# Kernel optimization log

Hardware: AMD Instinct MI355X
Metric: run time of the kernel (lower is better)

## Reference

```python
import jax, jax.numpy as jnp
import numpy as np

# ---- config (mirrors cfg in __init__) ----
XB = (-51.2, 51.2, 0.2)
YB = (-51.2, 51.2, 0.2)
ZB = (-10.0, 10.0, 20.0)
C_BEV = 64
BN_EPS = 1e-5

DX = jnp.array([XB[2], YB[2], ZB[2]], jnp.float32)
BX = jnp.array([XB[0] + XB[2] / 2, YB[0] + YB[2] / 2, ZB[0] + ZB[2] / 2], jnp.float32)
NX = (int((XB[1] - XB[0]) / XB[2]), int((YB[1] - YB[0]) / YB[2]), int((ZB[1] - ZB[0]) / ZB[2]))  # (512, 512, 1)


def setup_inputs() -> dict:
    key = jax.random.key(0)
    k1, k2, k3, k4 = jax.random.split(key, 4)
    B, N = 4, 100000
    xy = jax.random.uniform(k1, (B, N, 2), jnp.float32, -54.0, 54.0)   # some points out of bounds
    z = jax.random.uniform(k2, (B, N, 1), jnp.float32, -3.0, 3.0)
    inten = jax.random.uniform(k3, (B, N, 1), jnp.float32)
    points = jnp.concatenate([xy, z, inten], axis=-1)
    W = jax.random.normal(k4, (4, C_BEV), jnp.float32) * 0.5
    b = jnp.zeros((C_BEV,), jnp.float32)
    gamma = jnp.ones((C_BEV,), jnp.float32)
    beta = jnp.zeros((C_BEV,), jnp.float32)
    return {"points": points, "W": W, "b": b, "gamma": gamma, "beta": beta}


def reference(points, W, b, gamma, beta):
    B, N, _ = points.shape
    nx, ny, nz = NX
    p = points.reshape(-1, 4)                      # (B*N, 4)

    # PFN: Linear + BatchNorm1d (training-mode batch stats, biased var) + ReLU
    h = p @ W + b                                  # (B*N, C)
    mu = jnp.mean(h, axis=0)
    var = jnp.var(h, axis=0)
    feat = jax.nn.relu(gamma * (h - mu) * jax.lax.rsqrt(var + BN_EPS) + beta)

    # grid coords: torch .long() truncates toward zero; jnp astype(int) does too
    coords = ((p[:, :3] - (BX - DX / 2.0)) / DX).astype(jnp.int32)
    kept = ((coords[:, 0] >= 0) & (coords[:, 0] < nx)
            & (coords[:, 1] >= 0) & (coords[:, 1] < ny)
            & (coords[:, 2] >= 0) & (coords[:, 2] < nz))

    batch_ix = jnp.repeat(jnp.arange(B, dtype=jnp.int32), N)
    ranks = (batch_ix * (nx * ny * nz)
             + coords[:, 0] + coords[:, 1] * nx + coords[:, 2] * (nx * ny))

    # invalid points -> sentinel bucket (jit-safe replacement for boolean filtering).
    # segment_sum per unique rank == the sort + QuickCumsum trick + scatter-assign.
    flat = B * nx * ny * nz
    ranks = jnp.where(kept, ranks, flat)
    feat = jnp.where(kept[:, None], feat, 0.0)
    bev = jax.ops.segment_sum(feat, ranks, num_segments=flat + 1)[:flat]  # (flat, C)

    bev = bev.reshape(B, nz, ny, nx, C_BEV)
    bev = jnp.transpose(bev, (0, 4, 1, 2, 3)).sum(axis=2)  # (B, C, ny, nx)
    return bev
```

## Files before the change

### kernel.cpp

```cpp
#include <hip/hip_runtime.h>


#define NXG 512
#define NYXG (512 * 512)
#define CB 64
#define SBLK 256
#define YCH 16
#define CAP 384

typedef float f32x4 __attribute__((ext_vector_type(4)));

__device__ __forceinline__ int coord_mul5(float x, float offx) {
    float t = x - offx;
    asm volatile("" : "+v"(t));
    float q = t * 5.0f;
    asm volatile("" : "+v"(q));
    return (int)q;
}

__global__ void zero_ints(int* __restrict__ p, int n) {
    int i = blockIdx.x * blockDim.x + threadIdx.x;
    if (i < n) p[i] = 0;
}

__global__ void zero_kernel(float4* __restrict__ p, long n4) {
    long i = (long)blockIdx.x * blockDim.x + threadIdx.x;
    long stride = (long)gridDim.x * blockDim.x;
    float4 z = make_float4(0.f, 0.f, 0.f, 0.f);
    for (; i < n4; i += stride) p[i] = z;
}

__global__ void stats_reorder(const float4* __restrict__ pts, const float* __restrict__ W,
                              double* __restrict__ S_part, int* __restrict__ cursor,
                              float4* __restrict__ pts_s, int M, int Nper) {
    __shared__ float4 tile[256];
    __shared__ double sh1[256], sh2[256];
    int t = threadIdx.x;
    int lane = t & 63;
    int wv = t >> 6;
    float w0 = W[lane], w1 = W[64 + lane], w2 = W[128 + lane], w3 = W[192 + lane];
    const float offx = -51.1f - 0.1f;
    double s1 = 0.0, s2 = 0.0;

    int chunk = (M + gridDim.x - 1) / gridDim.x;
    int base = blockIdx.x * chunk;
    int end = base + chunk; if (end > M) end = M;

    for (int i0 = base; i0 < end; i0 += 256) {
        int n = end - i0; if (n > 256) n = 256;
        __syncthreads();
        if (t < n) {
            float4 p = pts[i0 + t];
            tile[t] = p;
            int cx = coord_mul5(p.x, offx);
            int cy = coord_mul5(p.y, offx);
            if (cx >= 0 && cx < NXG && cy >= 0 && cy < NXG) {
                int b = (i0 + t) / Nper;
                int row = (b << 9) | cy;
                int idx = atomicAdd(&cursor[row], 1);
                if (idx < CAP) pts_s[(size_t)row * CAP + idx] = p;
            }
        }
        __syncthreads();
        int j0 = wv * 64, j1 = j0 + 64; if (j1 > n) j1 = n;
        for (int j = j0; j < j1; ++j) {
            float4 p = tile[j];
            float q = p.x * w0 + p.y * w1 + p.z * w2 + p.w * w3;
            double qd = (double)q;
            s1 += qd;
            s2 += qd * qd;
        }
    }
    sh1[t] = s1;
    sh2[t] = s2;
    __syncthreads();
    if (t < 64) {
        int c = t;
        S_part[(long)blockIdx.x * 128 + c] =
            (sh1[c] + sh1[64 + c]) + (sh1[128 + c] + sh1[192 + c]);
        S_part[(long)blockIdx.x * 128 + 64 + c] =
            (sh2[c] + sh2[64 + c]) + (sh2[128 + c] + sh2[192 + c]);
    }
}

__global__ void reduce_finalize(const double* __restrict__ S_part,
                                const float* __restrict__ gamma, const float* __restrict__ beta,
                                float* __restrict__ AB, double invM) {
    __shared__ double sh[4][128];
    __shared__ double tot[128];
    int t = threadIdx.x;
    int g = t >> 7, tt = t & 127;
    const double* base = S_part + (long)g * 64 * 128 + tt;
    double a0 = 0.0, a1 = 0.0, a2 = 0.0, a3 = 0.0;
#pragma unroll
    for (int b = 0; b < 64; b += 4) {
        a0 += base[(long)(b + 0) * 128];
        a1 += base[(long)(b + 1) * 128];
        a2 += base[(long)(b + 2) * 128];
        a3 += base[(long)(b + 3) * 128];
    }
    sh[g][tt] = (a0 + a1) + (a2 + a3);
    __syncthreads();
    if (t < 128) tot[t] = (sh[0][t] + sh[1][t]) + (sh[2][t] + sh[3][t]);
    __syncthreads();
    if (t < 64) {
        double mu = tot[t] * invM;
        double var = tot[64 + t] * invM - mu * mu;
        double sc = (double)gamma[t] / sqrt(var + 1e-5);
        AB[t] = (float)sc;
        AB[64 + t] = (float)((double)beta[t] - mu * sc);
    }
}

__global__ __launch_bounds__(256) void gather_out(
    const float4* __restrict__ pts_s, const float* __restrict__ W,
    const float* __restrict__ AB, const int* __restrict__ cursor,
    float* __restrict__ out) {
    __shared__ float acc[YCH][NXG];
    __shared__ int cnts[YCH];
    int t = threadIdx.x;
    int c = blockIdx.x & 63;
    int yc = (blockIdx.x >> 6) & 31;
    int b = blockIdx.x >> 11;
    int rowbase = (b << 9) + (yc << 4);

    f32x4* az = (f32x4*)acc;
#pragma unroll
    for (int j = t; j < YCH * NXG / 4; j += 256) az[j] = (f32x4)(0.f);
    if (t < YCH) {
        int cc = cursor[rowbase + t];
        cnts[t] = cc > CAP ? CAP : cc;
    }

    float w0 = W[c], w1 = W[64 + c], w2 = W[128 + c], w3 = W[192 + c];
    float A = AB[c], Bc = AB[64 + c];
    const float offx = -51.1f - 0.1f;
    __syncthreads();

    for (int rr = 0; rr < YCH; ++rr) {
        int cnt = cnts[rr];
        const float4* src = pts_s + (size_t)(rowbase + rr) * CAP;
        for (int i = t; i < cnt; i += 256) {
            float4 p = src[i];
            int cx = coord_mul5(p.x, offx);
            float q = p.x * w0 + p.y * w1 + p.z * w2 + p.w * w3;
            float f = fmaxf(q * A + Bc, 0.f);
            atomicAdd(&acc[rr][cx], f);
        }
    }
    __syncthreads();

    f32x4* o4 = (f32x4*)(out + ((size_t)(b * CB + c) * NXG + (yc << 4)) * NXG);
#pragma unroll
    for (int j = t; j < YCH * NXG / 4; j += 256)
        __builtin_nontemporal_store(az[j], &o4[j]);
}

__global__ void stats_only(const float4* __restrict__ pts, const float* __restrict__ W,
                           double* __restrict__ S_part, int M) {
    __shared__ float4 tile[256];
    __shared__ double sh1[256], sh2[256];
    int t = threadIdx.x, lane = t & 63, wv = t >> 6;
    float w0 = W[lane], w1 = W[64 + lane], w2 = W[128 + lane], w3 = W[192 + lane];
    double s1 = 0.0, s2 = 0.0;
    int chunk = (M + gridDim.x - 1) / gridDim.x;
    int base = blockIdx.x * chunk;
    int end = base + chunk; if (end > M) end = M;
    for (int i0 = base; i0 < end; i0 += 256) {
        int n = end - i0; if (n > 256) n = 256;
        __syncthreads();
        if (t < n) tile[t] = pts[i0 + t];
        __syncthreads();
        int j0 = wv * 64, j1 = j0 + 64; if (j1 > n) j1 = n;
        for (int j = j0; j < j1; ++j) {
            float4 p = tile[j];
            float q = p.x * w0 + p.y * w1 + p.z * w2 + p.w * w3;
            double qd = (double)q;
            s1 += qd; s2 += qd * qd;
        }
    }
    sh1[t] = s1; sh2[t] = s2;
    __syncthreads();
    if (t < 64) {
        int c = t;
        S_part[(long)blockIdx.x * 128 + c] =
            (sh1[c] + sh1[64 + c]) + (sh1[128 + c] + sh1[192 + c]);
        S_part[(long)blockIdx.x * 128 + 64 + c] =
            (sh2[c] + sh2[64 + c]) + (sh2[128 + c] + sh2[192 + c]);
    }
}

__global__ void scatter_direct(const float4* __restrict__ pts, const float* __restrict__ W,
                               const float* __restrict__ AB, float* __restrict__ out,
                               int M, int Nper) {
    int lane = threadIdx.x & 63;
    int wid = blockIdx.x * (blockDim.x >> 6) + (threadIdx.x >> 6);
    int nw = gridDim.x * (blockDim.x >> 6);
    float w0 = W[lane], w1 = W[64 + lane], w2 = W[128 + lane], w3 = W[192 + lane];
    float A = AB[lane], Bc = AB[64 + lane];
    const float offx = -51.1f - 0.1f;
    for (int i = wid; i < M; i += nw) {
        float4 p = pts[i];
        int cx = coord_mul5(p.x, offx);
        int cy = coord_mul5(p.y, offx);
        if (cx < 0 || cx >= NXG || cy < 0 || cy >= NXG) continue;
        int b = i / Nper;
        float q = p.x * w0 + p.y * w1 + p.z * w2 + p.w * w3;
        float f = fmaxf(q * A + Bc, 0.f);
        atomicAdd(&out[((long)(b * CB + lane) * NXG + cy) * NXG + cx], f);
    }
}

extern "C" void kernel_launch(void* const* d_in, const int* in_sizes, int n_in,
                              void* d_out, int out_size, void* d_ws, size_t ws_size,
                              hipStream_t stream) {
    const float4* pts = (const float4*)d_in[0];
    const float* W = (const float*)d_in[1];
    const float* gamma = (const float*)d_in[3];
    const float* beta = (const float*)d_in[4];
    float* out = (float*)d_out;

    int M = in_sizes[0] / 4;
    int B = out_size / (CB * NYXG);
    int Nper = M / B;
    int NROWS = B * 512;

    char* wsb = (char*)d_ws;
    float* AB = (float*)(wsb + 1024);
    double* S_part = (double*)(wsb + 2048);

    size_t off = 2048 + (size_t)SBLK * 128 * sizeof(double);
    int* cursor = (int*)(wsb + off);     off += (size_t)NROWS * 4;
    off = (off + 255) & ~(size_t)255;
    float4* pts_s = (float4*)(wsb + off);
    off += (size_t)NROWS * CAP * 16;
    size_t need = off;

    if (ws_size >= need) {
        zero_ints<<<(NROWS + 255) / 256, 256, 0, stream>>>(cursor, NROWS);
        stats_reorder<<<SBLK, 256, 0, stream>>>(pts, W, S_part, cursor, pts_s, M, Nper);
        reduce_finalize<<<1, 512, 0, stream>>>(S_part, gamma, beta, AB, 1.0 / (double)M);
        gather_out<<<B * 32 * 64, 256, 0, stream>>>(pts_s, W, AB, cursor, out);
    } else {
        zero_kernel<<<2048, 256, 0, stream>>>((float4*)out, (long)out_size / 4);
        stats_only<<<SBLK, 256, 0, stream>>>(pts, W, S_part, M);
        reduce_finalize<<<1, 512, 0, stream>>>(S_part, gamma, beta, AB, 1.0 / (double)M);
        scatter_direct<<<2048, 256, 0, stream>>>(pts, W, AB, out, M, Nper);
    }
}
```

Baseline: 203.3 us.

## Compute BatchNorm stats from input moments instead of per-channel projections

```diff
diff --git a/kernel.cpp b/kernel.cpp
--- a/kernel.cpp
+++ b/kernel.cpp
@@ -4,7 +4,7 @@
 #define NXG 512
 #define NYXG (512 * 512)
 #define CB 64
-#define SBLK 256
+#define NST 512
 #define YCH 16
 #define CAP 384
 
@@ -30,82 +30,81 @@
     for (; i < n4; i += stride) p[i] = z;
 }
 
-__global__ void stats_reorder(const float4* __restrict__ pts, const float* __restrict__ W,
-                              double* __restrict__ S_part, int* __restrict__ cursor,
-                              float4* __restrict__ pts_s, int M, int Nper) {
-    __shared__ float4 tile[256];
-    __shared__ double sh1[256], sh2[256];
-    int t = threadIdx.x;
-    int lane = t & 63;
-    int wv = t >> 6;
-    float w0 = W[lane], w1 = W[64 + lane], w2 = W[128 + lane], w3 = W[192 + lane];
+__global__ __launch_bounds__(256) void stats_reorder(
+    const float4* __restrict__ pts, double* __restrict__ S_part,
+    int* __restrict__ cursor, float4* __restrict__ pts_s, int M, int Nper) {
+    double mm[14];
+#pragma unroll
+    for (int v = 0; v < 14; ++v) mm[v] = 0.0;
+
     const float offx = -51.1f - 0.1f;
-    double s1 = 0.0, s2 = 0.0;
-
-    int chunk = (M + gridDim.x - 1) / gridDim.x;
-    int base = blockIdx.x * chunk;
-    int end = base + chunk; if (end > M) end = M;
-
-    for (int i0 = base; i0 < end; i0 += 256) {
-        int n = end - i0; if (n > 256) n = 256;
-        __syncthreads();
-        if (t < n) {
-            float4 p = pts[i0 + t];
-            tile[t] = p;
-            int cx = coord_mul5(p.x, offx);
-            int cy = coord_mul5(p.y, offx);
-            if (cx >= 0 && cx < NXG && cy >= 0 && cy < NXG) {
-                int b = (i0 + t) / Nper;
-                int row = (b << 9) | cy;
-                int idx = atomicAdd(&cursor[row], 1);
-                if (idx < CAP) pts_s[(size_t)row * CAP + idx] = p;
-            }
+    int i = blockIdx.x * blockDim.x + threadIdx.x;
+    int stride = gridDim.x * blockDim.x;
+    for (; i < M; i += stride) {
+        float4 p = pts[i];
+        int cx = coord_mul5(p.x, offx);
+        int cy = coord_mul5(p.y, offx);
+        if (cx >= 0 && cx < NXG && cy >= 0 && cy < NXG) {
+            int b = i / Nper;
+            int row = (b << 9) | cy;
+            int idx = atomicAdd(&cursor[row], 1);
+            if (idx < CAP) pts_s[(size_t)row * CAP + idx] = p;
         }
-        __syncthreads();
-        int j0 = wv * 64, j1 = j0 + 64; if (j1 > n) j1 = n;
-        for (int j = j0; j < j1; ++j) {
-            float4 p = tile[j];
-            float q = p.x * w0 + p.y * w1 + p.z * w2 + p.w * w3;
-            double qd = (double)q;
-            s1 += qd;
-            s2 += qd * qd;
-        }
-    }
-    sh1[t] = s1;
-    sh2[t] = s2;
+        double x = p.x, y = p.y, z = p.z, w = p.w;
+        mm[0] += x; mm[1] += y; mm[2] += z; mm[3] += w;
+        mm[4] += x * x; mm[5] += x * y; mm[6] += x * z; mm[7] += x * w;
+        mm[8] += y * y; mm[9] += y * z; mm[10] += y * w;
+        mm[11] += z * z; mm[12] += z * w; mm[13] += w * w;
+    }
+
+#pragma unroll
+    for (int o = 32; o > 0; o >>= 1) {
+#pragma unroll
+        for (int v = 0; v < 14; ++v) mm[v] += __shfl_down(mm[v], o);
+    }
+    __shared__ double sh[4][14];
+    int lane = threadIdx.x & 63, wv = threadIdx.x >> 6;
+    if (lane == 0) {
+#pragma unroll
+        for (int v = 0; v < 14; ++v) sh[wv][v] = mm[v];
+    }
+    __syncthreads();
+    int t = threadIdx.x;
+    if (t < 14)
+        S_part[(long)blockIdx.x * 16 + t] =
+            (sh[0][t] + sh[1][t]) + (sh[2][t] + sh[3][t]);
+}
+
+__global__ void reduce_finalize(const double* __restrict__ S_part,
+                                const float* __restrict__ W,
+                                const float* __restrict__ gamma, const float* __restrict__ beta,
+                                float* __restrict__ AB, double invM, int nparts) {
+    __shared__ double sh[14][16];
+    __shared__ double tot[14];
+    int t = threadIdx.x;
+    if (t < 224) {
+        int v = t >> 4, s = t & 15;
+        double a = 0.0;
+        for (int k = s; k < nparts; k += 16) a += S_part[(long)k * 16 + v];
+        sh[v][s] = a;
+    }
+    __syncthreads();
+    if (t < 14) {
+        double a = 0.0;
+#pragma unroll
+        for (int s = 0; s < 16; ++s) a += sh[t][s];
+        tot[t] = a;
+    }
     __syncthreads();
     if (t < 64) {
-        int c = t;
-        S_part[(long)blockIdx.x * 128 + c] =
-            (sh1[c] + sh1[64 + c]) + (sh1[128 + c] + sh1[192 + c]);
-        S_part[(long)blockIdx.x * 128 + 64 + c] =
-            (sh2[c] + sh2[64 + c]) + (sh2[128 + c] + sh2[192 + c]);
-    }
-}
-
-__global__ void reduce_finalize(const double* __restrict__ S_part,
-                                const float* __restrict__ gamma, const float* __restrict__ beta,
-                                float* __restrict__ AB, double invM) {
-    __shared__ double sh[4][128];
-    __shared__ double tot[128];
-    int t = threadIdx.x;
-    int g = t >> 7, tt = t & 127;
-    const double* base = S_part + (long)g * 64 * 128 + tt;
-    double a0 = 0.0, a1 = 0.0, a2 = 0.0, a3 = 0.0;
-#pragma unroll
-    for (int b = 0; b < 64; b += 4) {
-        a0 += base[(long)(b + 0) * 128];
-        a1 += base[(long)(b + 1) * 128];
-        a2 += base[(long)(b + 2) * 128];
-        a3 += base[(long)(b + 3) * 128];
-    }
-    sh[g][tt] = (a0 + a1) + (a2 + a3);
-    __syncthreads();
-    if (t < 128) tot[t] = (sh[0][t] + sh[1][t]) + (sh[2][t] + sh[3][t]);
-    __syncthreads();
-    if (t < 64) {
-        double mu = tot[t] * invM;
-        double var = tot[64 + t] * invM - mu * mu;
+        double w0 = W[t], w1 = W[64 + t], w2 = W[128 + t], w3 = W[192 + t];
+        double mu = (tot[0] * w0 + tot[1] * w1 + tot[2] * w2 + tot[3] * w3) * invM;
+        double e2 = (w0 * w0 * tot[4] + w1 * w1 * tot[8]
+                   + w2 * w2 * tot[11] + w3 * w3 * tot[13]
+                   + 2.0 * (w0 * w1 * tot[5] + w0 * w2 * tot[6] + w0 * w3 * tot[7]
+                          + w1 * w2 * tot[9] + w1 * w3 * tot[10] + w2 * w3 * tot[12]))
+                  * invM;
+        double var = e2 - mu * mu;
         double sc = (double)gamma[t] / sqrt(var + 1e-5);
         AB[t] = (float)sc;
         AB[64 + t] = (float)((double)beta[t] - mu * sc);
@@ -156,38 +155,37 @@
         __builtin_nontemporal_store(az[j], &o4[j]);
 }
 
-__global__ void stats_only(const float4* __restrict__ pts, const float* __restrict__ W,
-                           double* __restrict__ S_part, int M) {
-    __shared__ float4 tile[256];
-    __shared__ double sh1[256], sh2[256];
-    int t = threadIdx.x, lane = t & 63, wv = t >> 6;
-    float w0 = W[lane], w1 = W[64 + lane], w2 = W[128 + lane], w3 = W[192 + lane];
-    double s1 = 0.0, s2 = 0.0;
-    int chunk = (M + gridDim.x - 1) / gridDim.x;
-    int base = blockIdx.x * chunk;
-    int end = base + chunk; if (end > M) end = M;
-    for (int i0 = base; i0 < end; i0 += 256) {
-        int n = end - i0; if (n > 256) n = 256;
-        __syncthreads();
-        if (t < n) tile[t] = pts[i0 + t];
-        __syncthreads();
-        int j0 = wv * 64, j1 = j0 + 64; if (j1 > n) j1 = n;
-        for (int j = j0; j < j1; ++j) {
-            float4 p = tile[j];
-            float q = p.x * w0 + p.y * w1 + p.z * w2 + p.w * w3;
-            double qd = (double)q;
-            s1 += qd; s2 += qd * qd;
-        }
-    }
-    sh1[t] = s1; sh2[t] = s2;
-    __syncthreads();
-    if (t < 64) {
-        int c = t;
-        S_part[(long)blockIdx.x * 128 + c] =
-            (sh1[c] + sh1[64 + c]) + (sh1[128 + c] + sh1[192 + c]);
-        S_part[(long)blockIdx.x * 128 + 64 + c] =
-            (sh2[c] + sh2[64 + c]) + (sh2[128 + c] + sh2[192 + c]);
-    }
+__global__ __launch_bounds__(256) void stats_only(
+    const float4* __restrict__ pts, double* __restrict__ S_part, int M) {
+    double mm[14];
+#pragma unroll
+    for (int v = 0; v < 14; ++v) mm[v] = 0.0;
+    int i = blockIdx.x * blockDim.x + threadIdx.x;
+    int stride = gridDim.x * blockDim.x;
+    for (; i < M; i += stride) {
+        float4 p = pts[i];
+        double x = p.x, y = p.y, z = p.z, w = p.w;
+        mm[0] += x; mm[1] += y; mm[2] += z; mm[3] += w;
+        mm[4] += x * x; mm[5] += x * y; mm[6] += x * z; mm[7] += x * w;
+        mm[8] += y * y; mm[9] += y * z; mm[10] += y * w;
+        mm[11] += z * z; mm[12] += z * w; mm[13] += w * w;
+    }
+#pragma unroll
+    for (int o = 32; o > 0; o >>= 1) {
+#pragma unroll
+        for (int v = 0; v < 14; ++v) mm[v] += __shfl_down(mm[v], o);
+    }
+    __shared__ double sh[4][14];
+    int lane = threadIdx.x & 63, wv = threadIdx.x >> 6;
+    if (lane == 0) {
+#pragma unroll
+        for (int v = 0; v < 14; ++v) sh[wv][v] = mm[v];
+    }
+    __syncthreads();
+    int t = threadIdx.x;
+    if (t < 14)
+        S_part[(long)blockIdx.x * 16 + t] =
+            (sh[0][t] + sh[1][t]) + (sh[2][t] + sh[3][t]);
 }
 
 __global__ void scatter_direct(const float4* __restrict__ pts, const float* __restrict__ W,
@@ -229,7 +227,7 @@
     float* AB = (float*)(wsb + 1024);
     double* S_part = (double*)(wsb + 2048);
 
-    size_t off = 2048 + (size_t)SBLK * 128 * sizeof(double);
+    size_t off = 2048 + (size_t)NST * 16 * sizeof(double);
     int* cursor = (int*)(wsb + off);     off += (size_t)NROWS * 4;
     off = (off + 255) & ~(size_t)255;
     float4* pts_s = (float4*)(wsb + off);
@@ -238,13 +236,15 @@
 
     if (ws_size >= need) {
         zero_ints<<<(NROWS + 255) / 256, 256, 0, stream>>>(cursor, NROWS);
-        stats_reorder<<<SBLK, 256, 0, stream>>>(pts, W, S_part, cursor, pts_s, M, Nper);
-        reduce_finalize<<<1, 512, 0, stream>>>(S_part, gamma, beta, AB, 1.0 / (double)M);
+        stats_reorder<<<NST, 256, 0, stream>>>(pts, S_part, cursor, pts_s, M, Nper);
+        reduce_finalize<<<1, 256, 0, stream>>>(S_part, W, gamma, beta, AB,
+                                               1.0 / (double)M, NST);
         gather_out<<<B * 32 * 64, 256, 0, stream>>>(pts_s, W, AB, cursor, out);
     } else {
         zero_kernel<<<2048, 256, 0, stream>>>((float4*)out, (long)out_size / 4);
-        stats_only<<<SBLK, 256, 0, stream>>>(pts, W, S_part, M);
-        reduce_finalize<<<1, 512, 0, stream>>>(S_part, gamma, beta, AB, 1.0 / (double)M);
+        stats_only<<<NST, 256, 0, stream>>>(pts, S_part, M);
+        reduce_finalize<<<1, 256, 0, stream>>>(S_part, W, gamma, beta, AB,
+                                               1.0 / (double)M, NST);
         scatter_direct<<<2048, 256, 0, stream>>>(pts, W, AB, out, M, Nper);
     }
 }
```

Result: slower. 227.1 us (+11.7%).
